# Kernel tuning notes

Hardware: AMD Instinct MI355X
Metric: run time of the kernel (lower is better)

The kernel has to match this reference:

```python
import jax, jax.numpy as jnp
import numpy as np

B, T, DD, NS, V, E, H, L = 8192, 200, 8, 4, 1000, 32, 256, 2


def setup_inputs() -> dict:
    key = jax.random.key(0)
    ks = jax.random.split(key, 10)
    s = 0.05
    dense = jax.random.normal(ks[0], (B, T, DD), jnp.float32)
    sparse = jax.random.randint(ks[1], (B, T, NS), 0, V)
    lengths = jax.random.randint(ks[2], (B,), 1, T + 1)
    emb_tables = jax.random.normal(ks[3], (NS, V, E), jnp.float32) * s
    Wl = jax.random.normal(ks[4], (H, DD + NS * E), jnp.float32) * s
    bl = jnp.zeros((H,), jnp.float32)
    # axis1: 0 = rnn_entry_exit (even t), 1 = rnn_exit_entry (odd t)
    Wih = jax.random.normal(ks[5], (L, 2, H, H), jnp.float32) * s
    Whh = jax.random.normal(ks[6], (L, 2, H, H), jnp.float32) * s
    bih = jnp.zeros((L, 2, H), jnp.float32)
    bhh = jnp.zeros((L, 2, H), jnp.float32)
    Wout = jax.random.normal(ks[7], (1, H), jnp.float32) * s
    bout = jnp.zeros((1,), jnp.float32)
    return dict(dense=dense, sparse=sparse, lengths=lengths, emb_tables=emb_tables,
                Wl=Wl, bl=bl, Wih=Wih, Whh=Whh, bih=bih, bhh=bhh, Wout=Wout, bout=bout)


def reference(dense, sparse, lengths, emb_tables, Wl, bl, Wih, Whh, bih, bhh, Wout, bout):
    # Padded+mask formulation; equivalent to the packed-sequence loop:
    # finished sequences' hidden states are frozen (== being sliced away),
    # and the final frozen h of the top layer is the per-sequence output.
    # Dropout is identity (eval mode); it is never applied in forward anyway.
    mask = jnp.arange(T)[None, :] < lengths[:, None]        # [B, T]
    d_t = jnp.swapaxes(dense, 0, 1)                          # [T, B, DD]
    s_t = jnp.swapaxes(sparse, 0, 1)                         # [T, B, NS]
    m_t = mask.T                                             # [T, B]

    def embed(st):  # [B, NS] -> [B, NS*E], matching torch.cat of per-feature embeddings
        e = jax.vmap(lambda tab, idx: tab[idx], in_axes=(0, 1), out_axes=1)(emb_tables, st)
        return e.reshape(st.shape[0], NS * E)

    def step(h, xs):  # h: [L, B, H]
        t, dt, st, mt = xs
        x = jnp.concatenate([dt, embed(st)], axis=-1)        # [B, DD+NS*E]
        x = jax.nn.relu(x @ Wl.T + bl)                       # [B, H]
        p = t % 2                                            # which cell set this step
        hs = []
        for i in range(L):
            hn = jnp.tanh(x @ Wih[i, p].T + bih[i, p] + h[i] @ Whh[i, p].T + bhh[i, p])
            hi = jnp.where(mt[:, None], hn, h[i])
            hs.append(hi)
            x = hi
        return jnp.stack(hs), None

    h0 = jnp.zeros((L, B, H), dense.dtype)
    hT, _ = jax.lax.scan(step, h0, (jnp.arange(T), d_t, s_t, m_t))
    return jax.nn.sigmoid(hT[-1] @ Wout.T + bout)[:, 0]     # [B]
```

## Files before the change

kernel.cpp:

```cpp
#include <hip/hip_runtime.h>
#include <math.h>


typedef __attribute__((ext_vector_type(8))) short bf16x8;
typedef __attribute__((ext_vector_type(4))) short s16x4;
typedef __attribute__((ext_vector_type(4))) float f32x4;

#define MFMA(a, b, c) __builtin_amdgcn_mfma_f32_16x16x32_bf16((a), (b), (c), 0, 0, 0)

#define T_  200

#define WLP_OFF   0
#define WIHP_OFF  40960
#define WHHP_OFF  (40960 + 262144)
#define BSUM_BYTE_OFF ((40960 + 262144 + 262144) * 2)

#define XCS 168
#define HS  264
#define SM_XCAT 0
#define SM_XPJ  5376
#define SM_H0   (SM_XPJ + 8448)
#define SM_H1A  (SM_H0 + 8448)
#define SM_H1B  (SM_H1A + 8448)
#define SM_BIAS (SM_H1B + 8448)
#define SM_TOT  (SM_BIAS + 2560)

__device__ __forceinline__ short f2bf(float f) {
    unsigned u = __float_as_uint(f);
    u += 0x7fffu + ((u >> 16) & 1u);
    return (short)(u >> 16);
}
__device__ __forceinline__ float bf2f(short s) {
    return __uint_as_float(((unsigned)(unsigned short)s) << 16);
}
__device__ __forceinline__ float tanh_fast(float x) {
    float e = __builtin_amdgcn_exp2f(x * 2.88539008f);
    return 1.0f - 2.0f * __builtin_amdgcn_rcpf(e + 1.0f);
}

__global__ void prep_kernel(const float* __restrict__ Wl,
                            const float* __restrict__ Wih,
                            const float* __restrict__ Whh,
                            const float* __restrict__ bih,
                            const float* __restrict__ bhh,
                            short* __restrict__ wsS,
                            float* __restrict__ bsum) {
    int tid = blockIdx.x * 256 + threadIdx.x;
    if (tid < 5120) {
        int mt = tid / 320, rem = tid % 320;
        int kk = rem / 64, lane = rem % 64;
        int o = mt * 16 + (lane & 15);
        int kb = kk * 32 + (lane >> 4) * 8;
        short* dst = wsS + WLP_OFF + tid * 8;
#pragma unroll
        for (int e = 0; e < 8; e++) {
            int k = kb + e;
            dst[e] = f2bf((k < 136) ? Wl[o * 136 + k] : 0.0f);
        }
    } else if (tid < 5120 + 32768) {
        int jj = tid - 5120;
        int mat = jj / 8192, rem = jj % 8192;
        int lane = rem & 63, kk = (rem >> 6) & 7, mt = rem >> 9;
        int o = mt * 16 + (lane & 15);
        int kb = kk * 32 + (lane >> 4) * 8;
        const float* src = Wih + (mat * 256 + o) * 256;
        short* dst = wsS + WIHP_OFF + mat * 65536 + rem * 8;
#pragma unroll
        for (int e = 0; e < 8; e++) dst[e] = f2bf(src[kb + e]);
    } else if (tid < 5120 + 65536) {
        int jj = tid - 37888;
        int mat = jj / 8192, rem = jj % 8192;
        int lane = rem & 63, kk = (rem >> 6) & 7, mt = rem >> 9;
        int o = mt * 16 + (lane & 15);
        int kb = kk * 32 + (lane >> 4) * 8;
        const float* src = Whh + (mat * 256 + o) * 256;
        short* dst = wsS + WHHP_OFF + mat * 65536 + rem * 8;
#pragma unroll
        for (int e = 0; e < 8; e++) dst[e] = f2bf(src[kb + e]);
    } else if (tid < 5120 + 65536 + 1024) {
        int j = tid - 70656;
        bsum[j] = bih[j] + bhh[j];
    }
}

struct GReg { f32x4 e0, e1, dv; };

__device__ __forceinline__ void gather_load(GReg& g, const float* __restrict__ dense,
                                            const int* __restrict__ sparse,
                                            const float* __restrict__ emb,
                                            int b0, int tt, int tid) {
    int gs = tid >> 4, gf = (tid >> 2) & 3, gq = tid & 3;
    int ix = sparse[(b0 + gs) * (T_ * 4) + tt * 4 + gf];
    const float* ep = emb + gf * 32000 + ix * 32 + gq * 8;
    g.e0 = *(const f32x4*)ep;
    g.e1 = *(const f32x4*)(ep + 4);
    if (tid < 64)
        g.dv = *(const f32x4*)(dense + (b0 + (tid >> 1)) * (T_ * 8) + tt * 8 + (tid & 1) * 4);
}
__device__ __forceinline__ void gather_commit(const GReg& g, short* __restrict__ buf, int tid) {
    int gs = tid >> 4, gf = (tid >> 2) & 3, gq = tid & 3;
    s16x4 w0, w1;
#pragma unroll
    for (int r = 0; r < 4; r++) { w0[r] = f2bf(g.e0[r]); w1[r] = f2bf(g.e1[r]); }
    int off = gs * XCS + 8 + gf * 32 + gq * 8;
    *(s16x4*)(buf + off) = w0;
    *(s16x4*)(buf + off + 4) = w1;
    if (tid < 64) {
        s16x4 wd;
#pragma unroll
        for (int r = 0; r < 4; r++) wd[r] = f2bf(g.dv[r]);
        *(s16x4*)(buf + (tid >> 1) * XCS + (tid & 1) * 4) = wd;
    }
}

__device__ __forceinline__ void load_c4(bf16x8 (&d)[4], const short* A, const short* B,
                                        int kk, int wid, int lane) {
    d[0] = *(const bf16x8*)(A + (((wid * 2 + 0) * 8 + kk) * 64 + lane) * 8);
    d[1] = *(const bf16x8*)(A + (((wid * 2 + 1) * 8 + kk) * 64 + lane) * 8);
    d[2] = *(const bf16x8*)(B + (((wid * 2 + 0) * 8 + kk) * 64 + lane) * 8);
    d[3] = *(const bf16x8*)(B + (((wid * 2 + 1) * 8 + kk) * 64 + lane) * 8);
}
__device__ __forceinline__ void load_wl2(bf16x8& d0, bf16x8& d1,
                                         const short* Wlp, int kk, int wid, int lane) {
    d0 = *(const bf16x8*)(Wlp + (((wid * 2 + 0) * 5 + kk) * 64 + lane) * 8);
    d1 = *(const bf16x8*)(Wlp + (((wid * 2 + 1) * 5 + kk) * 64 + lane) * 8);
}

__global__ __launch_bounds__(512, 1) void rnn_kernel(
    const float* __restrict__ dense, const int* __restrict__ sparse,
    const int* __restrict__ lengths, const float* __restrict__ emb,
    const float* __restrict__ bl, const float* __restrict__ Wout,
    const float* __restrict__ bout, const short* __restrict__ wsS,
    const float* __restrict__ bsum, float* __restrict__ out) {
    __shared__ alignas(16) short sm[SM_TOT];
    short* xcat = sm + SM_XCAT;
    short* xpj  = sm + SM_XPJ;
    short* h0p  = sm + SM_H0;
    short* h1a  = sm + SM_H1A;
    short* h1b  = sm + SM_H1B;
    float* blS  = (float*)(sm + SM_BIAS);

    const int tid  = threadIdx.x;
    const int wid  = tid >> 6;
    const int lane = tid & 63;
    const int lrow = lane & 15;
    const int lgrp = lane >> 4;
    const int b0   = blockIdx.x * 32;
    const short* Wlp = wsS + WLP_OFF;

    for (int i = tid; i < SM_BIAS; i += 512) sm[i] = 0;
    for (int i = tid; i < 1280; i += 512)
        blS[i] = (i < 256) ? bl[i] : bsum[i - 256];

    const int len0 = lengths[b0 + lrow];
    const int len1 = lengths[b0 + 16 + lrow];

    __syncthreads();
    { GReg g0; gather_load(g0, dense, sparse, emb, b0, 0, tid); gather_commit(g0, xcat, tid); }
    __syncthreads();

    {
        f32x4 xacc[2][2];
#pragma unroll
        for (int mt = 0; mt < 2; mt++) {
            f32x4 bi = *(const f32x4*)(blS + wid * 32 + mt * 16 + lgrp * 4);
            xacc[mt][0] = bi; xacc[mt][1] = bi;
        }
#pragma unroll
        for (int kk = 0; kk < 5; kk++) {
            bf16x8 wl0, wl1;
            load_wl2(wl0, wl1, Wlp, kk, wid, lane);
            bf16x8 bxf[2];
#pragma unroll
            for (int nt = 0; nt < 2; nt++)
                bxf[nt] = *(const bf16x8*)(xcat + (nt * 16 + lrow) * XCS + kk * 32 + lgrp * 8);
#pragma unroll
            for (int nt = 0; nt < 2; nt++) {
                xacc[0][nt] = MFMA(wl0, bxf[nt], xacc[0][nt]);
                xacc[1][nt] = MFMA(wl1, bxf[nt], xacc[1][nt]);
            }
        }
#pragma unroll
        for (int mt = 0; mt < 2; mt++) {
            int o0 = wid * 32 + mt * 16 + lgrp * 4;
#pragma unroll
            for (int nt = 0; nt < 2; nt++) {
                s16x4 w;
#pragma unroll
                for (int r = 0; r < 4; r++) w[r] = f2bf(fmaxf(xacc[mt][nt][r], 0.0f));
                *(s16x4*)(xpj + (nt * 16 + lrow) * HS + o0) = w;
            }
        }
    }

    bf16x8 wa[3][4];
    bf16x8 wnext[4];
    bf16x8 hreg0[2][8];
#pragma unroll
    for (int nt = 0; nt < 2; nt++)
#pragma unroll
        for (int kk = 0; kk < 8; kk++) {
            bf16x8 z;
#pragma unroll
            for (int e = 0; e < 8; e++) z[e] = 0;
            hreg0[nt][kk] = z;
        }

    load_c4(wa[0], wsS + WIHP_OFF, wsS + WHHP_OFF, 0, wid, lane);
    load_c4(wa[1], wsS + WIHP_OFF, wsS + WHHP_OFF, 1, wid, lane);
    GReg g;
    gather_load(g, dense, sparse, emb, b0, 1, tid);
    __syncthreads();

    f32x4 acc[2][2];

    for (int t = 0; t < T_; t++) {
        const int p = t & 1;
        const bool hasNext = (t + 1 < T_);
        const short* Aih1 = wsS + WIHP_OFF + p * 65536;
        const short* Ahh1 = wsS + WHHP_OFF + p * 65536;
        const short* Aih2 = wsS + WIHP_OFF + (2 + p) * 65536;
        const short* Ahh2 = wsS + WHHP_OFF + (2 + p) * 65536;
        const short* AihN = wsS + WIHP_OFF + (p ^ 1) * 65536;
        const short* AhhN = wsS + WHHP_OFF + (p ^ 1) * 65536;

#pragma unroll
        for (int mt = 0; mt < 2; mt++) {
            f32x4 bi = *(const f32x4*)(blS + 256 + p * 256 + wid * 32 + mt * 16 + lgrp * 4);
            acc[mt][0] = bi; acc[mt][1] = bi;
        }
#pragma unroll
        for (int kk = 0; kk < 8; kk++) {
            if (kk <= 5)      load_c4(wa[(kk + 2) % 3], Aih1, Ahh1, kk + 2, wid, lane);
            else if (kk == 6) load_c4(wnext, Aih2, Ahh2, 0, wid, lane);
            else              load_c4(wa[2], Aih2, Ahh2, 1, wid, lane);
            const int s = kk % 3;
            bf16x8 bxf[2];
#pragma unroll
            for (int nt = 0; nt < 2; nt++)
                bxf[nt] = *(const bf16x8*)(xpj + (nt * 16 + lrow) * HS + kk * 32 + lgrp * 8);
#pragma unroll
            for (int mt = 0; mt < 2; mt++)
#pragma unroll
                for (int nt = 0; nt < 2; nt++) {
                    acc[mt][nt] = MFMA(wa[s][mt], bxf[nt], acc[mt][nt]);
                    acc[mt][nt] = MFMA(wa[s][2 + mt], hreg0[nt][kk], acc[mt][nt]);
                }
        }
#pragma unroll
        for (int mt = 0; mt < 2; mt++) {
            int o0 = wid * 32 + mt * 16 + lgrp * 4;
#pragma unroll
            for (int nt = 0; nt < 2; nt++) {
                s16x4 w;
#pragma unroll
                for (int r = 0; r < 4; r++) w[r] = f2bf(tanh_fast(acc[mt][nt][r]));
                int len = nt ? len1 : len0;
                if (t < len)
                    *(s16x4*)(h0p + (nt * 16 + lrow) * HS + o0) = w;
            }
        }
        if (hasNext) gather_commit(g, xcat, tid);
        __syncthreads();

        const short* h1r = p ? h1b : h1a;
        short* h1w = p ? h1a : h1b;
#pragma unroll
        for (int mt = 0; mt < 2; mt++) {
            f32x4 bi = *(const f32x4*)(blS + 256 + (2 + p) * 256 + wid * 32 + mt * 16 + lgrp * 4);
            acc[mt][0] = bi; acc[mt][1] = bi;
        }
#pragma unroll
        for (int kk = 0; kk < 8; kk++) {
            if (kk <= 5)      load_c4(wa[kk % 3], Aih2, Ahh2, kk + 2, wid, lane);
            else if (kk == 6) { if (hasNext) load_wl2(wnext[0], wnext[1], Wlp, 0, wid, lane); }
            else              { if (hasNext) load_wl2(wnext[2], wnext[3], Wlp, 1, wid, lane); }
            bf16x8 bhf[2];
#pragma unroll
            for (int nt = 0; nt < 2; nt++) {
                hreg0[nt][kk] = *(const bf16x8*)(h0p + (nt * 16 + lrow) * HS + kk * 32 + lgrp * 8);
                bhf[nt] = *(const bf16x8*)(h1r + (nt * 16 + lrow) * HS + kk * 32 + lgrp * 8);
            }
            if (kk == 0) {
#pragma unroll
                for (int mt = 0; mt < 2; mt++)
#pragma unroll
                    for (int nt = 0; nt < 2; nt++) {
                        acc[mt][nt] = MFMA(wnext[mt], hreg0[nt][0], acc[mt][nt]);
                        acc[mt][nt] = MFMA(wnext[2 + mt], bhf[nt], acc[mt][nt]);
                    }
            } else {
                const int s = (kk + 1) % 3;
#pragma unroll
                for (int mt = 0; mt < 2; mt++)
#pragma unroll
                    for (int nt = 0; nt < 2; nt++) {
                        acc[mt][nt] = MFMA(wa[s][mt], hreg0[nt][kk], acc[mt][nt]);
                        acc[mt][nt] = MFMA(wa[s][2 + mt], bhf[nt], acc[mt][nt]);
                    }
            }
        }
#pragma unroll
        for (int mt = 0; mt < 2; mt++) {
            int o0 = wid * 32 + mt * 16 + lgrp * 4;
#pragma unroll
            for (int nt = 0; nt < 2; nt++) {
                int roff = (nt * 16 + lrow) * HS + o0;
                s16x4 oldv = *(const s16x4*)(h1r + roff);
                s16x4 w;
#pragma unroll
                for (int r = 0; r < 4; r++) w[r] = f2bf(tanh_fast(acc[mt][nt][r]));
                int len = nt ? len1 : len0;
                *(s16x4*)(h1w + roff) = (t < len) ? w : oldv;
            }
        }

        if (hasNext) {
#pragma unroll
            for (int mt = 0; mt < 2; mt++) {
                f32x4 bi = *(const f32x4*)(blS + wid * 32 + mt * 16 + lgrp * 4);
                acc[mt][0] = bi; acc[mt][1] = bi;
            }
#pragma unroll
            for (int kk = 0; kk < 5; kk++) {
                if (kk <= 2)      load_wl2(wa[kk][0], wa[kk][1], Wlp, kk + 2, wid, lane);
                else if (kk == 3) load_c4(wa[0], AihN, AhhN, 0, wid, lane);
                else              load_c4(wa[1], AihN, AhhN, 1, wid, lane);
                bf16x8 w0, w1;
                if (kk == 0)      { w0 = wnext[0]; w1 = wnext[1]; }
                else if (kk == 1) { w0 = wnext[2]; w1 = wnext[3]; }
                else              { w0 = wa[kk - 2][0]; w1 = wa[kk - 2][1]; }
                bf16x8 bxf[2];
#pragma unroll
                for (int nt = 0; nt < 2; nt++)
                    bxf[nt] = *(const bf16x8*)(xcat + (nt * 16 + lrow) * XCS + kk * 32 + lgrp * 8);
#pragma unroll
                for (int nt = 0; nt < 2; nt++) {
                    acc[0][nt] = MFMA(w0, bxf[nt], acc[0][nt]);
                    acc[1][nt] = MFMA(w1, bxf[nt], acc[1][nt]);
                }
            }
#pragma unroll
            for (int mt = 0; mt < 2; mt++) {
                int o0 = wid * 32 + mt * 16 + lgrp * 4;
#pragma unroll
                for (int nt = 0; nt < 2; nt++) {
                    s16x4 w;
#pragma unroll
                    for (int r = 0; r < 4; r++) w[r] = f2bf(fmaxf(acc[mt][nt][r], 0.0f));
                    *(s16x4*)(xpj + (nt * 16 + lrow) * HS + o0) = w;
                }
            }
            if (t + 2 < T_)
                gather_load(g, dense, sparse, emb, b0, t + 2, tid);
        }
        __syncthreads();
    }

    float* red = (float*)(sm + SM_XPJ);
    if (tid < 256) {
        int s = tid >> 3, part = tid & 7;
        const short* hr = h1a + s * HS + part * 32;
        float sum = 0.0f;
#pragma unroll
        for (int k = 0; k < 32; k++) sum += bf2f(hr[k]) * Wout[part * 32 + k];
        red[s * 8 + part] = sum;
    }
    __syncthreads();
    if (tid < 32) {
        float x = bout[0];
#pragma unroll
        for (int i = 0; i < 8; i++) x += red[tid * 8 + i];
        float e = __builtin_amdgcn_exp2f(x * 1.44269504f);
        out[b0 + tid] = 1.0f - __builtin_amdgcn_rcpf(1.0f + e);
    }
}

extern "C" void kernel_launch(void* const* d_in, const int* in_sizes, int n_in,
                              void* d_out, int out_size, void* d_ws, size_t ws_size,
                              hipStream_t stream) {
    const float* dense   = (const float*)d_in[0];
    const int*   sparse  = (const int*)d_in[1];
    const int*   lengths = (const int*)d_in[2];
    const float* emb     = (const float*)d_in[3];
    const float* Wl      = (const float*)d_in[4];
    const float* bl      = (const float*)d_in[5];
    const float* Wih     = (const float*)d_in[6];
    const float* Whh     = (const float*)d_in[7];
    const float* bih     = (const float*)d_in[8];
    const float* bhh     = (const float*)d_in[9];
    const float* Wout    = (const float*)d_in[10];
    const float* bout    = (const float*)d_in[11];

    short* wsS  = (short*)d_ws;
    float* bsum = (float*)((char*)d_ws + BSUM_BYTE_OFF);

    prep_kernel<<<280, 256, 0, stream>>>(Wl, Wih, Whh, bih, bhh, wsS, bsum);
    rnn_kernel<<<256, 512, 0, stream>>>(dense, sparse, lengths, emb, bl, Wout, bout,
                                        wsS, bsum, (float*)d_out);
}
```

Before: 1.157 ms.

## Stage Wl in LDS, deepen weight prefetch, and defer layer-1 hidden writeback

The input projection weight Wl is now copied once into shared memory and read from LDS each step, so it no longer competes with the global loads of the RNN weights. The Wih/Whh prefetch is restructured to keep three k-slices in flight and to issue each load after the MFMAs that use the current slice. The layer-1 hidden state is held in registers and written to a single LDS buffer at the start of the next step, replacing the double-buffered read-old/write-new masking. This raises LDS use to about 148KB and adds register pressure, which may cost occupancy or cause spills.

```diff
diff --git a/kernel.cpp b/kernel.cpp
--- a/kernel.cpp
+++ b/kernel.cpp
@@ -19,11 +19,11 @@
 #define HS  264
 #define SM_XCAT 0
 #define SM_XPJ  5376
-#define SM_H0   (SM_XPJ + 8448)
-#define SM_H1A  (SM_H0 + 8448)
-#define SM_H1B  (SM_H1A + 8448)
-#define SM_BIAS (SM_H1B + 8448)
-#define SM_TOT  (SM_BIAS + 2560)
+#define SM_H0   (5376 + 8448)
+#define SM_H1   (13824 + 8448)
+#define SM_WL   (22272 + 8448)
+#define SM_BIAS (30720 + 40960)
+#define SM_TOT  (71680 + 2560)
 
 __device__ __forceinline__ short f2bf(float f) {
     unsigned u = __float_as_uint(f);
@@ -120,11 +120,6 @@
     d[2] = *(const bf16x8*)(B + (((wid * 2 + 0) * 8 + kk) * 64 + lane) * 8);
     d[3] = *(const bf16x8*)(B + (((wid * 2 + 1) * 8 + kk) * 64 + lane) * 8);
 }
-__device__ __forceinline__ void load_wl2(bf16x8& d0, bf16x8& d1,
-                                         const short* Wlp, int kk, int wid, int lane) {
-    d0 = *(const bf16x8*)(Wlp + (((wid * 2 + 0) * 5 + kk) * 64 + lane) * 8);
-    d1 = *(const bf16x8*)(Wlp + (((wid * 2 + 1) * 5 + kk) * 64 + lane) * 8);
-}
 
 __global__ __launch_bounds__(512, 1) void rnn_kernel(
     const float* __restrict__ dense, const int* __restrict__ sparse,
@@ -136,8 +131,8 @@
     short* xcat = sm + SM_XCAT;
     short* xpj  = sm + SM_XPJ;
     short* h0p  = sm + SM_H0;
-    short* h1a  = sm + SM_H1A;
-    short* h1b  = sm + SM_H1B;
+    short* h1p  = sm + SM_H1;
+    short* wlS  = sm + SM_WL;
     float* blS  = (float*)(sm + SM_BIAS);
 
     const int tid  = threadIdx.x;
@@ -146,9 +141,10 @@
     const int lrow = lane & 15;
     const int lgrp = lane >> 4;
     const int b0   = blockIdx.x * 32;
-    const short* Wlp = wsS + WLP_OFF;
-
-    for (int i = tid; i < SM_BIAS; i += 512) sm[i] = 0;
+
+    for (int i = tid; i < SM_WL; i += 512) sm[i] = 0;
+    for (int i = tid; i < 5120; i += 512)
+        ((bf16x8*)wlS)[i] = ((const bf16x8*)(wsS + WLP_OFF))[i];
     for (int i = tid; i < 1280; i += 512)
         blS[i] = (i < 256) ? bl[i] : bsum[i - 256];
 
@@ -168,8 +164,8 @@
         }
 #pragma unroll
         for (int kk = 0; kk < 5; kk++) {
-            bf16x8 wl0, wl1;
-            load_wl2(wl0, wl1, Wlp, kk, wid, lane);
+            bf16x8 wl0 = *(const bf16x8*)(wlS + (((wid * 2 + 0) * 5 + kk) * 64 + lane) * 8);
+            bf16x8 wl1 = *(const bf16x8*)(wlS + (((wid * 2 + 1) * 5 + kk) * 64 + lane) * 8);
             bf16x8 bxf[2];
 #pragma unroll
             for (int nt = 0; nt < 2; nt++)
@@ -196,6 +192,7 @@
     bf16x8 wa[3][4];
     bf16x8 wnext[4];
     bf16x8 hreg0[2][8];
+    s16x4  h1def[2][2];
 #pragma unroll
     for (int nt = 0; nt < 2; nt++)
 #pragma unroll
@@ -205,9 +202,14 @@
             for (int e = 0; e < 8; e++) z[e] = 0;
             hreg0[nt][kk] = z;
         }
+#pragma unroll
+    for (int mt = 0; mt < 2; mt++)
+#pragma unroll
+        for (int nt = 0; nt < 2; nt++) { s16x4 z; z[0]=z[1]=z[2]=z[3]=0; h1def[mt][nt] = z; }
 
     load_c4(wa[0], wsS + WIHP_OFF, wsS + WHHP_OFF, 0, wid, lane);
     load_c4(wa[1], wsS + WIHP_OFF, wsS + WHHP_OFF, 1, wid, lane);
+    load_c4(wa[2], wsS + WIHP_OFF, wsS + WHHP_OFF, 2, wid, lane);
     GReg g;
     gather_load(g, dense, sparse, emb, b0, 1, tid);
     __syncthreads();
@@ -224,6 +226,19 @@
         const short* AihN = wsS + WIHP_OFF + (p ^ 1) * 65536;
         const short* AhhN = wsS + WHHP_OFF + (p ^ 1) * 65536;
 
+        if (t > 0) {
+#pragma unroll
+            for (int mt = 0; mt < 2; mt++) {
+                int o0 = wid * 32 + mt * 16 + lgrp * 4;
+#pragma unroll
+                for (int nt = 0; nt < 2; nt++) {
+                    int len = nt ? len1 : len0;
+                    if (t - 1 < len)
+                        *(s16x4*)(h1p + (nt * 16 + lrow) * HS + o0) = h1def[mt][nt];
+                }
+            }
+        }
+
 #pragma unroll
         for (int mt = 0; mt < 2; mt++) {
             f32x4 bi = *(const f32x4*)(blS + 256 + p * 256 + wid * 32 + mt * 16 + lgrp * 4);
@@ -231,9 +246,6 @@
         }
 #pragma unroll
         for (int kk = 0; kk < 8; kk++) {
-            if (kk <= 5)      load_c4(wa[(kk + 2) % 3], Aih1, Ahh1, kk + 2, wid, lane);
-            else if (kk == 6) load_c4(wnext, Aih2, Ahh2, 0, wid, lane);
-            else              load_c4(wa[2], Aih2, Ahh2, 1, wid, lane);
             const int s = kk % 3;
             bf16x8 bxf[2];
 #pragma unroll
@@ -246,6 +258,10 @@
                     acc[mt][nt] = MFMA(wa[s][mt], bxf[nt], acc[mt][nt]);
                     acc[mt][nt] = MFMA(wa[s][2 + mt], hreg0[nt][kk], acc[mt][nt]);
                 }
+            if (kk <= 4)      load_c4(wa[s], Aih1, Ahh1, kk + 3, wid, lane);
+            else if (kk == 5) load_c4(wnext, Aih2, Ahh2, 0, wid, lane);
+            else if (kk == 6) load_c4(wa[2], Aih2, Ahh2, 1, wid, lane);
+            else              load_c4(wa[0], Aih2, Ahh2, 2, wid, lane);
         }
 #pragma unroll
         for (int mt = 0; mt < 2; mt++) {
@@ -263,8 +279,6 @@
         if (hasNext) gather_commit(g, xcat, tid);
         __syncthreads();
 
-        const short* h1r = p ? h1b : h1a;
-        short* h1w = p ? h1a : h1b;
 #pragma unroll
         for (int mt = 0; mt < 2; mt++) {
             f32x4 bi = *(const f32x4*)(blS + 256 + (2 + p) * 256 + wid * 32 + mt * 16 + lgrp * 4);
@@ -272,14 +286,11 @@
         }
 #pragma unroll
         for (int kk = 0; kk < 8; kk++) {
-            if (kk <= 5)      load_c4(wa[kk % 3], Aih2, Ahh2, kk + 2, wid, lane);
-            else if (kk == 6) { if (hasNext) load_wl2(wnext[0], wnext[1], Wlp, 0, wid, lane); }
-            else              { if (hasNext) load_wl2(wnext[2], wnext[3], Wlp, 1, wid, lane); }
             bf16x8 bhf[2];
 #pragma unroll
             for (int nt = 0; nt < 2; nt++) {
                 hreg0[nt][kk] = *(const bf16x8*)(h0p + (nt * 16 + lrow) * HS + kk * 32 + lgrp * 8);
-                bhf[nt] = *(const bf16x8*)(h1r + (nt * 16 + lrow) * HS + kk * 32 + lgrp * 8);
+                bhf[nt] = *(const bf16x8*)(h1p + (nt * 16 + lrow) * HS + kk * 32 + lgrp * 8);
             }
             if (kk == 0) {
 #pragma unroll
@@ -299,21 +310,23 @@
                         acc[mt][nt] = MFMA(wa[s][2 + mt], bhf[nt], acc[mt][nt]);
                     }
             }
-        }
-#pragma unroll
-        for (int mt = 0; mt < 2; mt++) {
-            int o0 = wid * 32 + mt * 16 + lgrp * 4;
+            if (kk == 0)      load_c4(wa[1], Aih2, Ahh2, 3, wid, lane);
+            else if (kk <= 4) load_c4(wa[(kk + 1) % 3], Aih2, Ahh2, kk + 3, wid, lane);
+            else if (hasNext) {
+                if (kk == 5)      load_c4(wa[0], AihN, AhhN, 0, wid, lane);
+                else if (kk == 6) load_c4(wa[1], AihN, AhhN, 1, wid, lane);
+                else              load_c4(wa[2], AihN, AhhN, 2, wid, lane);
+            }
+        }
+#pragma unroll
+        for (int mt = 0; mt < 2; mt++)
 #pragma unroll
             for (int nt = 0; nt < 2; nt++) {
-                int roff = (nt * 16 + lrow) * HS + o0;
-                s16x4 oldv = *(const s16x4*)(h1r + roff);
                 s16x4 w;
 #pragma unroll
                 for (int r = 0; r < 4; r++) w[r] = f2bf(tanh_fast(acc[mt][nt][r]));
-                int len = nt ? len1 : len0;
-                *(s16x4*)(h1w + roff) = (t < len) ? w : oldv;
-            }
-        }
+                h1def[mt][nt] = w;
+            }
 
         if (hasNext) {
 #pragma unroll
@@ -323,21 +336,16 @@
             }
 #pragma unroll
             for (int kk = 0; kk < 5; kk++) {
-                if (kk <= 2)      load_wl2(wa[kk][0], wa[kk][1], Wlp, kk + 2, wid, lane);
-                else if (kk == 3) load_c4(wa[0], AihN, AhhN, 0, wid, lane);
-                else              load_c4(wa[1], AihN, AhhN, 1, wid, lane);
-                bf16x8 w0, w1;
-                if (kk == 0)      { w0 = wnext[0]; w1 = wnext[1]; }
-                else if (kk == 1) { w0 = wnext[2]; w1 = wnext[3]; }
-                else              { w0 = wa[kk - 2][0]; w1 = wa[kk - 2][1]; }
+                bf16x8 wl0 = *(const bf16x8*)(wlS + (((wid * 2 + 0) * 5 + kk) * 64 + lane) * 8);
+                bf16x8 wl1 = *(const bf16x8*)(wlS + (((wid * 2 + 1) * 5 + kk) * 64 + lane) * 8);
                 bf16x8 bxf[2];
 #pragma unroll
                 for (int nt = 0; nt < 2; nt++)
                     bxf[nt] = *(const bf16x8*)(xcat + (nt * 16 + lrow) * XCS + kk * 32 + lgrp * 8);
 #pragma unroll
                 for (int nt = 0; nt < 2; nt++) {
-                    acc[0][nt] = MFMA(w0, bxf[nt], acc[0][nt]);
-                    acc[1][nt] = MFMA(w1, bxf[nt], acc[1][nt]);
+                    acc[0][nt] = MFMA(wl0, bxf[nt], acc[0][nt]);
+                    acc[1][nt] = MFMA(wl1, bxf[nt], acc[1][nt]);
                 }
             }
 #pragma unroll
@@ -357,10 +365,22 @@
         __syncthreads();
     }
 
+#pragma unroll
+    for (int mt = 0; mt < 2; mt++) {
+        int o0 = wid * 32 + mt * 16 + lgrp * 4;
+#pragma unroll
+        for (int nt = 0; nt < 2; nt++) {
+            int len = nt ? len1 : len0;
+            if (T_ - 1 < len)
+                *(s16x4*)(h1p + (nt * 16 + lrow) * HS + o0) = h1def[mt][nt];
+        }
+    }
+    __syncthreads();
+
     float* red = (float*)(sm + SM_XPJ);
     if (tid < 256) {
         int s = tid >> 3, part = tid & 7;
-        const short* hr = h1a + s * HS + part * 32;
+        const short* hr = h1p + s * HS + part * 32;
         float sum = 0.0f;
 #pragma unroll
         for (int k = 0; k < 32; k++) sum += bf2f(hr[k]) * Wout[part * 32 + k];
```

Result: slower. 1.276 ms (+10.3%).

## Single-buffer layer-1 hidden state with deferred register writeback and unrolled parity

Applied to the files above, without the earlier changes.

The double-buffered layer-1 hidden state in shared memory becomes a single buffer. Each step's new layer-1 outputs stay in registers and are written to shared memory at the start of the next step, after the barrier, which removes the per-step read of the old value for masking. The time loop is also unrolled by two through a template on parity, so the weight-slice pointer offsets become compile-time constants. This frees shared memory and a few instructions, at the cost of extra live registers and a final flush before the output reduction.

```diff
diff --git a/kernel.cpp b/kernel.cpp
--- a/kernel.cpp
+++ b/kernel.cpp
@@ -19,11 +19,10 @@
 #define HS  264
 #define SM_XCAT 0
 #define SM_XPJ  5376
-#define SM_H0   (SM_XPJ + 8448)
-#define SM_H1A  (SM_H0 + 8448)
-#define SM_H1B  (SM_H1A + 8448)
-#define SM_BIAS (SM_H1B + 8448)
-#define SM_TOT  (SM_BIAS + 2560)
+#define SM_H0   (5376 + 8448)
+#define SM_H1   (13824 + 8448)
+#define SM_BIAS (22272 + 8448)
+#define SM_TOT  (30720 + 2560)
 
 __device__ __forceinline__ short f2bf(float f) {
     unsigned u = __float_as_uint(f);
@@ -126,6 +125,167 @@
     d1 = *(const bf16x8*)(Wlp + (((wid * 2 + 1) * 5 + kk) * 64 + lane) * 8);
 }
 
+template<int P>
+__device__ __forceinline__ void rnn_step(
+    int t, bool hasNext,
+    const float* __restrict__ dense, const int* __restrict__ sparse,
+    const float* __restrict__ emb, const short* __restrict__ wsS,
+    const float* __restrict__ blS,
+    short* __restrict__ xcat, short* __restrict__ xpj,
+    short* __restrict__ h0p, short* __restrict__ h1p,
+    bf16x8 (&wa)[3][4], bf16x8 (&wnext)[4], bf16x8 (&hreg0)[2][8],
+    s16x4 (&h1def)[2][2], GReg& g,
+    int lane, int lrow, int lgrp, int wid, int len0, int len1, int b0, int tid)
+{
+    const short* Aih1 = wsS + WIHP_OFF + P * 65536;
+    const short* Ahh1 = wsS + WHHP_OFF + P * 65536;
+    const short* Aih2 = wsS + WIHP_OFF + (2 + P) * 65536;
+    const short* Ahh2 = wsS + WHHP_OFF + (2 + P) * 65536;
+    const short* AihN = wsS + WIHP_OFF + (P ^ 1) * 65536;
+    const short* AhhN = wsS + WHHP_OFF + (P ^ 1) * 65536;
+    const short* Wlp  = wsS + WLP_OFF;
+
+    f32x4 acc[2][2];
+
+    if (t > 0) {
+#pragma unroll
+        for (int mt = 0; mt < 2; mt++) {
+            int o0 = wid * 32 + mt * 16 + lgrp * 4;
+#pragma unroll
+            for (int nt = 0; nt < 2; nt++) {
+                int len = nt ? len1 : len0;
+                if (t - 1 < len)
+                    *(s16x4*)(h1p + (nt * 16 + lrow) * HS + o0) = h1def[mt][nt];
+            }
+        }
+    }
+
+#pragma unroll
+    for (int mt = 0; mt < 2; mt++) {
+        f32x4 bi = *(const f32x4*)(blS + 256 + P * 256 + wid * 32 + mt * 16 + lgrp * 4);
+        acc[mt][0] = bi; acc[mt][1] = bi;
+    }
+#pragma unroll
+    for (int kk = 0; kk < 8; kk++) {
+        if (kk <= 5)      load_c4(wa[(kk + 2) % 3], Aih1, Ahh1, kk + 2, wid, lane);
+        else if (kk == 6) load_c4(wnext, Aih2, Ahh2, 0, wid, lane);
+        else              load_c4(wa[2], Aih2, Ahh2, 1, wid, lane);
+        const int s = kk % 3;
+        bf16x8 bxf[2];
+#pragma unroll
+        for (int nt = 0; nt < 2; nt++)
+            bxf[nt] = *(const bf16x8*)(xpj + (nt * 16 + lrow) * HS + kk * 32 + lgrp * 8);
+#pragma unroll
+        for (int mt = 0; mt < 2; mt++)
+#pragma unroll
+            for (int nt = 0; nt < 2; nt++) {
+                acc[mt][nt] = MFMA(wa[s][mt], bxf[nt], acc[mt][nt]);
+                acc[mt][nt] = MFMA(wa[s][2 + mt], hreg0[nt][kk], acc[mt][nt]);
+            }
+    }
+#pragma unroll
+    for (int mt = 0; mt < 2; mt++) {
+        int o0 = wid * 32 + mt * 16 + lgrp * 4;
+#pragma unroll
+        for (int nt = 0; nt < 2; nt++) {
+            s16x4 w;
+#pragma unroll
+            for (int r = 0; r < 4; r++) w[r] = f2bf(tanh_fast(acc[mt][nt][r]));
+            int len = nt ? len1 : len0;
+            if (t < len)
+                *(s16x4*)(h0p + (nt * 16 + lrow) * HS + o0) = w;
+        }
+    }
+    if (hasNext) gather_commit(g, xcat, tid);
+    __syncthreads();
+
+#pragma unroll
+    for (int mt = 0; mt < 2; mt++) {
+        f32x4 bi = *(const f32x4*)(blS + 256 + (2 + P) * 256 + wid * 32 + mt * 16 + lgrp * 4);
+        acc[mt][0] = bi; acc[mt][1] = bi;
+    }
+#pragma unroll
+    for (int kk = 0; kk < 8; kk++) {
+        if (kk <= 5)      load_c4(wa[kk % 3], Aih2, Ahh2, kk + 2, wid, lane);
+        else if (kk == 6) { if (hasNext) load_wl2(wnext[0], wnext[1], Wlp, 0, wid, lane); }
+        else              { if (hasNext) load_wl2(wnext[2], wnext[3], Wlp, 1, wid, lane); }
+        bf16x8 bhf[2];
+#pragma unroll
+        for (int nt = 0; nt < 2; nt++) {
+            hreg0[nt][kk] = *(const bf16x8*)(h0p + (nt * 16 + lrow) * HS + kk * 32 + lgrp * 8);
+            bhf[nt] = *(const bf16x8*)(h1p + (nt * 16 + lrow) * HS + kk * 32 + lgrp * 8);
+        }
+        if (kk == 0) {
+#pragma unroll
+            for (int mt = 0; mt < 2; mt++)
+#pragma unroll
+                for (int nt = 0; nt < 2; nt++) {
+                    acc[mt][nt] = MFMA(wnext[mt], hreg0[nt][0], acc[mt][nt]);
+                    acc[mt][nt] = MFMA(wnext[2 + mt], bhf[nt], acc[mt][nt]);
+                }
+        } else {
+            const int s = (kk + 1) % 3;
+#pragma unroll
+            for (int mt = 0; mt < 2; mt++)
+#pragma unroll
+                for (int nt = 0; nt < 2; nt++) {
+                    acc[mt][nt] = MFMA(wa[s][mt], hreg0[nt][kk], acc[mt][nt]);
+                    acc[mt][nt] = MFMA(wa[s][2 + mt], bhf[nt], acc[mt][nt]);
+                }
+        }
+    }
+#pragma unroll
+    for (int mt = 0; mt < 2; mt++)
+#pragma unroll
+        for (int nt = 0; nt < 2; nt++) {
+            s16x4 w;
+#pragma unroll
+            for (int r = 0; r < 4; r++) w[r] = f2bf(tanh_fast(acc[mt][nt][r]));
+            h1def[mt][nt] = w;
+        }
+
+    if (hasNext) {
+#pragma unroll
+        for (int mt = 0; mt < 2; mt++) {
+            f32x4 bi = *(const f32x4*)(blS + wid * 32 + mt * 16 + lgrp * 4);
+            acc[mt][0] = bi; acc[mt][1] = bi;
+        }
+#pragma unroll
+        for (int kk = 0; kk < 5; kk++) {
+            if (kk <= 2)      load_wl2(wa[kk][0], wa[kk][1], Wlp, kk + 2, wid, lane);
+            else if (kk == 3) load_c4(wa[0], AihN, AhhN, 0, wid, lane);
+            else              load_c4(wa[1], AihN, AhhN, 1, wid, lane);
+            bf16x8 w0, w1;
+            if (kk == 0)      { w0 = wnext[0]; w1 = wnext[1]; }
+            else if (kk == 1) { w0 = wnext[2]; w1 = wnext[3]; }
+            else              { w0 = wa[kk - 2][0]; w1 = wa[kk - 2][1]; }
+            bf16x8 bxf[2];
+#pragma unroll
+            for (int nt = 0; nt < 2; nt++)
+                bxf[nt] = *(const bf16x8*)(xcat + (nt * 16 + lrow) * XCS + kk * 32 + lgrp * 8);
+#pragma unroll
+            for (int nt = 0; nt < 2; nt++) {
+                acc[0][nt] = MFMA(w0, bxf[nt], acc[0][nt]);
+                acc[1][nt] = MFMA(w1, bxf[nt], acc[1][nt]);
+            }
+        }
+#pragma unroll
+        for (int mt = 0; mt < 2; mt++) {
+            int o0 = wid * 32 + mt * 16 + lgrp * 4;
+#pragma unroll
+            for (int nt = 0; nt < 2; nt++) {
+                s16x4 w;
+#pragma unroll
+                for (int r = 0; r < 4; r++) w[r] = f2bf(fmaxf(acc[mt][nt][r], 0.0f));
+                *(s16x4*)(xpj + (nt * 16 + lrow) * HS + o0) = w;
+            }
+        }
+        if (t + 2 < T_)
+            gather_load(g, dense, sparse, emb, b0, t + 2, tid);
+    }
+    __syncthreads();
+}
+
 __global__ __launch_bounds__(512, 1) void rnn_kernel(
     const float* __restrict__ dense, const int* __restrict__ sparse,
     const int* __restrict__ lengths, const float* __restrict__ emb,
@@ -136,8 +296,7 @@
     short* xcat = sm + SM_XCAT;
     short* xpj  = sm + SM_XPJ;
     short* h0p  = sm + SM_H0;
-    short* h1a  = sm + SM_H1A;
-    short* h1b  = sm + SM_H1B;
+    short* h1p  = sm + SM_H1;
     float* blS  = (float*)(sm + SM_BIAS);
 
     const int tid  = threadIdx.x;
@@ -196,6 +355,7 @@
     bf16x8 wa[3][4];
     bf16x8 wnext[4];
     bf16x8 hreg0[2][8];
+    s16x4  h1def[2][2];
 #pragma unroll
     for (int nt = 0; nt < 2; nt++)
 #pragma unroll
@@ -205,6 +365,10 @@
             for (int e = 0; e < 8; e++) z[e] = 0;
             hreg0[nt][kk] = z;
         }
+#pragma unroll
+    for (int mt = 0; mt < 2; mt++)
+#pragma unroll
+        for (int nt = 0; nt < 2; nt++) { s16x4 z; z[0]=z[1]=z[2]=z[3]=0; h1def[mt][nt] = z; }
 
     load_c4(wa[0], wsS + WIHP_OFF, wsS + WHHP_OFF, 0, wid, lane);
     load_c4(wa[1], wsS + WIHP_OFF, wsS + WHHP_OFF, 1, wid, lane);
@@ -212,155 +376,31 @@
     gather_load(g, dense, sparse, emb, b0, 1, tid);
     __syncthreads();
 
-    f32x4 acc[2][2];
-
-    for (int t = 0; t < T_; t++) {
-        const int p = t & 1;
-        const bool hasNext = (t + 1 < T_);
-        const short* Aih1 = wsS + WIHP_OFF + p * 65536;
-        const short* Ahh1 = wsS + WHHP_OFF + p * 65536;
-        const short* Aih2 = wsS + WIHP_OFF + (2 + p) * 65536;
-        const short* Ahh2 = wsS + WHHP_OFF + (2 + p) * 65536;
-        const short* AihN = wsS + WIHP_OFF + (p ^ 1) * 65536;
-        const short* AhhN = wsS + WHHP_OFF + (p ^ 1) * 65536;
-
-#pragma unroll
-        for (int mt = 0; mt < 2; mt++) {
-            f32x4 bi = *(const f32x4*)(blS + 256 + p * 256 + wid * 32 + mt * 16 + lgrp * 4);
-            acc[mt][0] = bi; acc[mt][1] = bi;
-        }
-#pragma unroll
-        for (int kk = 0; kk < 8; kk++) {
-            if (kk <= 5)      load_c4(wa[(kk + 2) % 3], Aih1, Ahh1, kk + 2, wid, lane);
-            else if (kk == 6) load_c4(wnext, Aih2, Ahh2, 0, wid, lane);
-            else              load_c4(wa[2], Aih2, Ahh2, 1, wid, lane);
-            const int s = kk % 3;
-            bf16x8 bxf[2];
-#pragma unroll
-            for (int nt = 0; nt < 2; nt++)
-                bxf[nt] = *(const bf16x8*)(xpj + (nt * 16 + lrow) * HS + kk * 32 + lgrp * 8);
-#pragma unroll
-            for (int mt = 0; mt < 2; mt++)
-#pragma unroll
-                for (int nt = 0; nt < 2; nt++) {
-                    acc[mt][nt] = MFMA(wa[s][mt], bxf[nt], acc[mt][nt]);
-                    acc[mt][nt] = MFMA(wa[s][2 + mt], hreg0[nt][kk], acc[mt][nt]);
-                }
-        }
-#pragma unroll
-        for (int mt = 0; mt < 2; mt++) {
-            int o0 = wid * 32 + mt * 16 + lgrp * 4;
-#pragma unroll
-            for (int nt = 0; nt < 2; nt++) {
-                s16x4 w;
-#pragma unroll
-                for (int r = 0; r < 4; r++) w[r] = f2bf(tanh_fast(acc[mt][nt][r]));
-                int len = nt ? len1 : len0;
-                if (t < len)
-                    *(s16x4*)(h0p + (nt * 16 + lrow) * HS + o0) = w;
-            }
-        }
-        if (hasNext) gather_commit(g, xcat, tid);
-        __syncthreads();
-
-        const short* h1r = p ? h1b : h1a;
-        short* h1w = p ? h1a : h1b;
-#pragma unroll
-        for (int mt = 0; mt < 2; mt++) {
-            f32x4 bi = *(const f32x4*)(blS + 256 + (2 + p) * 256 + wid * 32 + mt * 16 + lgrp * 4);
-            acc[mt][0] = bi; acc[mt][1] = bi;
-        }
-#pragma unroll
-        for (int kk = 0; kk < 8; kk++) {
-            if (kk <= 5)      load_c4(wa[kk % 3], Aih2, Ahh2, kk + 2, wid, lane);
-            else if (kk == 6) { if (hasNext) load_wl2(wnext[0], wnext[1], Wlp, 0, wid, lane); }
-            else              { if (hasNext) load_wl2(wnext[2], wnext[3], Wlp, 1, wid, lane); }
-            bf16x8 bhf[2];
-#pragma unroll
-            for (int nt = 0; nt < 2; nt++) {
-                hreg0[nt][kk] = *(const bf16x8*)(h0p + (nt * 16 + lrow) * HS + kk * 32 + lgrp * 8);
-                bhf[nt] = *(const bf16x8*)(h1r + (nt * 16 + lrow) * HS + kk * 32 + lgrp * 8);
-            }
-            if (kk == 0) {
-#pragma unroll
-                for (int mt = 0; mt < 2; mt++)
-#pragma unroll
-                    for (int nt = 0; nt < 2; nt++) {
-                        acc[mt][nt] = MFMA(wnext[mt], hreg0[nt][0], acc[mt][nt]);
-                        acc[mt][nt] = MFMA(wnext[2 + mt], bhf[nt], acc[mt][nt]);
-                    }
-            } else {
-                const int s = (kk + 1) % 3;
-#pragma unroll
-                for (int mt = 0; mt < 2; mt++)
-#pragma unroll
-                    for (int nt = 0; nt < 2; nt++) {
-                        acc[mt][nt] = MFMA(wa[s][mt], hreg0[nt][kk], acc[mt][nt]);
-                        acc[mt][nt] = MFMA(wa[s][2 + mt], bhf[nt], acc[mt][nt]);
-                    }
-            }
-        }
-#pragma unroll
-        for (int mt = 0; mt < 2; mt++) {
-            int o0 = wid * 32 + mt * 16 + lgrp * 4;
-#pragma unroll
-            for (int nt = 0; nt < 2; nt++) {
-                int roff = (nt * 16 + lrow) * HS + o0;
-                s16x4 oldv = *(const s16x4*)(h1r + roff);
-                s16x4 w;
-#pragma unroll
-                for (int r = 0; r < 4; r++) w[r] = f2bf(tanh_fast(acc[mt][nt][r]));
-                int len = nt ? len1 : len0;
-                *(s16x4*)(h1w + roff) = (t < len) ? w : oldv;
-            }
-        }
-
-        if (hasNext) {
-#pragma unroll
-            for (int mt = 0; mt < 2; mt++) {
-                f32x4 bi = *(const f32x4*)(blS + wid * 32 + mt * 16 + lgrp * 4);
-                acc[mt][0] = bi; acc[mt][1] = bi;
-            }
-#pragma unroll
-            for (int kk = 0; kk < 5; kk++) {
-                if (kk <= 2)      load_wl2(wa[kk][0], wa[kk][1], Wlp, kk + 2, wid, lane);
-                else if (kk == 3) load_c4(wa[0], AihN, AhhN, 0, wid, lane);
-                else              load_c4(wa[1], AihN, AhhN, 1, wid, lane);
-                bf16x8 w0, w1;
-                if (kk == 0)      { w0 = wnext[0]; w1 = wnext[1]; }
-                else if (kk == 1) { w0 = wnext[2]; w1 = wnext[3]; }
-                else              { w0 = wa[kk - 2][0]; w1 = wa[kk - 2][1]; }
-                bf16x8 bxf[2];
-#pragma unroll
-                for (int nt = 0; nt < 2; nt++)
-                    bxf[nt] = *(const bf16x8*)(xcat + (nt * 16 + lrow) * XCS + kk * 32 + lgrp * 8);
-#pragma unroll
-                for (int nt = 0; nt < 2; nt++) {
-                    acc[0][nt] = MFMA(w0, bxf[nt], acc[0][nt]);
-                    acc[1][nt] = MFMA(w1, bxf[nt], acc[1][nt]);
-                }
-            }
-#pragma unroll
-            for (int mt = 0; mt < 2; mt++) {
-                int o0 = wid * 32 + mt * 16 + lgrp * 4;
-#pragma unroll
-                for (int nt = 0; nt < 2; nt++) {
-                    s16x4 w;
-#pragma unroll
-                    for (int r = 0; r < 4; r++) w[r] = f2bf(fmaxf(acc[mt][nt][r], 0.0f));
-                    *(s16x4*)(xpj + (nt * 16 + lrow) * HS + o0) = w;
-                }
-            }
-            if (t + 2 < T_)
-                gather_load(g, dense, sparse, emb, b0, t + 2, tid);
-        }
-        __syncthreads();
-    }
+    for (int tb = 0; tb < T_; tb += 2) {
+        rnn_step<0>(tb, true, dense, sparse, emb, wsS, blS, xcat, xpj, h0p, h1p,
+                    wa, wnext, hreg0, h1def, g,
+                    lane, lrow, lgrp, wid, len0, len1, b0, tid);
+        rnn_step<1>(tb + 1, tb + 1 < T_ - 1, dense, sparse, emb, wsS, blS,
+                    xcat, xpj, h0p, h1p, wa, wnext, hreg0, h1def, g,
+                    lane, lrow, lgrp, wid, len0, len1, b0, tid);
+    }
+
+#pragma unroll
+    for (int mt = 0; mt < 2; mt++) {
+        int o0 = wid * 32 + mt * 16 + lgrp * 4;
+#pragma unroll
+        for (int nt = 0; nt < 2; nt++) {
+            int len = nt ? len1 : len0;
+            if (T_ - 1 < len)
+                *(s16x4*)(h1p + (nt * 16 + lrow) * HS + o0) = h1def[mt][nt];
+        }
+    }
+    __syncthreads();
 
     float* red = (float*)(sm + SM_XPJ);
     if (tid < 256) {
         int s = tid >> 3, part = tid & 7;
-        const short* hr = h1a + s * HS + part * 32;
+        const short* hr = h1p + s * HS + part * 32;
         float sum = 0.0f;
 #pragma unroll
         for (int k = 0; k < 32; k++) sum += bf2f(hr[k]) * Wout[part * 32 + k];
```

Result: slower. 4.416 ms (+281.5%).
